# Kernel tuning notes

Measured on AMD Instinct MI355X. Metric: run time of the kernel, lower is better.

The kernel has to match this reference:

```python
import jax, jax.numpy as jnp
import numpy as np

B, S, D = 8, 1024, 1024
H = 16
DK = D // H  # 64, dim_k == dim_v
F = 4096
EPS = 1e-5


def _layernorm(x, w, b):
    mu = jnp.mean(x, axis=-1, keepdims=True)
    var = jnp.mean((x - mu) ** 2, axis=-1, keepdims=True)
    return (x - mu) * jax.lax.rsqrt(var + EPS) * w + b


def setup_inputs() -> dict:
    key = jax.random.key(0)
    ks = jax.random.split(key, 12)
    init = lambda k, shape: (jax.random.normal(k, shape, dtype=jnp.float32) * 0.02)
    return {
        "src": jax.random.normal(ks[0], (B, S, D), dtype=jnp.float32),
        "mask": jnp.zeros((S, S), dtype=jnp.float32),
        # per-head projections, stacked over heads: [H, D, DK]
        "Wq": init(ks[1], (H, D, DK)), "bq": jnp.zeros((H, DK), jnp.float32),
        "Wk": init(ks[2], (H, D, DK)), "bk": jnp.zeros((H, DK), jnp.float32),
        "Wv": init(ks[3], (H, D, DK)), "bv": jnp.zeros((H, DK), jnp.float32),
        "Wo": init(ks[4], (H * DK, D)), "bo": jnp.zeros((D,), jnp.float32),
        "ln1_w": jnp.ones((D,), jnp.float32), "ln1_b": jnp.zeros((D,), jnp.float32),
        "W1": init(ks[5], (D, F)), "b1": jnp.zeros((F,), jnp.float32),
        "W2": init(ks[6], (F, D)), "b2": jnp.zeros((D,), jnp.float32),
        "ln2_w": jnp.ones((D,), jnp.float32), "ln2_b": jnp.zeros((D,), jnp.float32),
    }


def reference(src, mask, Wq, bq, Wk, bk, Wv, bv, Wo, bo,
              ln1_w, ln1_b, W1, b1, W2, b2, ln2_w, ln2_b):
    # per-head projections (vectorized over heads): [B, H, S, DK]
    q = jnp.einsum('bsd,hdk->bhsk', src, Wq) + bq[None, :, None, :]
    k = jnp.einsum('bsd,hdk->bhsk', src, Wk) + bk[None, :, None, :]
    v = jnp.einsum('bsd,hdk->bhsk', src, Wv) + bv[None, :, None, :]
    scale = float(DK) ** 0.5
    logits = jnp.einsum('bhsk,bhtk->bhst', q, k) / scale  # [B,H,S,S]
    logits = logits + mask * (-1e9)
    attn = jax.nn.softmax(logits, axis=-1)
    ctx = jnp.einsum('bhst,bhtv->bhsv', attn, v)  # [B,H,S,DK]
    # concat heads along feature dim (head-major order matches torch cat)
    ctx = jnp.transpose(ctx, (0, 2, 1, 3)).reshape(B, S, H * DK)
    attn_out = ctx @ Wo + bo
    x = _layernorm(src + attn_out, ln1_w, ln1_b)
    ffn = jax.nn.relu(x @ W1 + b1) @ W2 + b2
    return _layernorm(x + ffn, ln2_w, ln2_b)
```

## Files before the change

### kernel.cpp

```cpp
#include <hip/hip_runtime.h>

#define BB 8
#define SS 1024
#define DD 1024
#define HH 16
#define DK 64
#define FF 4096
#define MM (BB*SS)

typedef __attribute__((ext_vector_type(8))) short short8;
typedef __attribute__((ext_vector_type(4))) short short4v;
typedef __attribute__((ext_vector_type(4))) float floatx4;

__device__ inline short f2bf(float f) {
  union { float f; unsigned u; } v; v.f = f;
  unsigned r = (v.u + 0x7FFFu + ((v.u >> 16) & 1u)) >> 16;
  return (short)r;
}
__device__ inline float bf2f(unsigned short u) {
  union { unsigned u; float f; } v; v.u = ((unsigned)u) << 16;
  return v.f;
}

__device__ inline void gload_lds16(const void* g, void* l) {
  __builtin_amdgcn_global_load_lds(
      (const __attribute__((address_space(1))) void*)g,
      (__attribute__((address_space(3))) void*)l, 16, 0, 0);
}

__device__ void tr64(const float* __restrict__ s, unsigned short* __restrict__ d,
                     int R, int C, int r0, int c0, float (*ld)[68], int tid) {
  {
    int r = tid >> 2, c16 = (tid & 3) * 16;
#pragma unroll
    for (int i = 0; i < 4; ++i)
      *(float4*)(&ld[r][c16 + i * 4]) =
          *(const float4*)(s + (size_t)(r0 + r) * C + c0 + c16 + i * 4);
  }
  __syncthreads();
  int c = tid >> 2, r16 = (tid & 3) * 16;
  short8 o0, o1;
#pragma unroll
  for (int i = 0; i < 8; ++i) {
    o0[i] = f2bf(ld[r16 + i][c]);
    o1[i] = f2bf(ld[r16 + 8 + i][c]);
  }
  unsigned short* dp = d + (size_t)(c0 + c) * R + r0 + r16;
  *(short8*)(dp) = o0;
  *(short8*)(dp + 8) = o1;
}

__global__ __launch_bounds__(256) void prep_all(
    const float* __restrict__ src,
    const float* __restrict__ Wq, const float* __restrict__ Wk,
    const float* __restrict__ Wv,
    const float* __restrict__ bq, const float* __restrict__ bk,
    const float* __restrict__ bv, const float* __restrict__ Wo,
    unsigned short* __restrict__ srcb, unsigned short* __restrict__ wqkvT,
    float* __restrict__ bqkv, unsigned short* __restrict__ woT) {
  __shared__ float ld[64][68];
  const int bid = blockIdx.x, tid = threadIdx.x;
  if (bid < 4096) {
    int i8 = (bid * 256 + tid) * 8;
    float4 a = *(const float4*)(src + i8);
    float4 b = *(const float4*)(src + i8 + 4);
    short8 o;
    o[0] = f2bf(a.x); o[1] = f2bf(a.y); o[2] = f2bf(a.z); o[3] = f2bf(a.w);
    o[4] = f2bf(b.x); o[5] = f2bf(b.y); o[6] = f2bf(b.z); o[7] = f2bf(b.w);
    *(short8*)(srcb + i8) = o;
  } else if (bid < 4864) {
    int idx = bid - 4096;
    int d0 = (idx & 15) * 64, h = (idx >> 4) & 15, z = idx >> 8;
    const float* W = (z == 0 ? Wq : z == 1 ? Wk : Wv) + (size_t)h * DD * DK;
    {
      int r = tid >> 2, c16 = (tid & 3) * 16;
#pragma unroll
      for (int i = 0; i < 4; ++i)
        *(float4*)(&ld[r][c16 + i * 4]) =
            *(const float4*)(W + (size_t)(d0 + r) * DK + c16 + i * 4);
    }
    __syncthreads();
    int dv = tid >> 2, d16 = (tid & 3) * 16;
    short8 o0, o1;
#pragma unroll
    for (int i = 0; i < 8; ++i) {
      o0[i] = f2bf(ld[d16 + i][dv]);
      o1[i] = f2bf(ld[d16 + 8 + i][dv]);
    }
    unsigned short* dst = wqkvT + (size_t)(z * 1024 + h * 64 + dv) * DD + d0 + d16;
    *(short8*)(dst) = o0;
    *(short8*)(dst + 8) = o1;
  } else if (bid < 4876) {
    int n = (bid - 4864) * 256 + tid;
    int z = n >> 10;
    const float* s = (z == 0 ? bq : z == 1 ? bk : bv);
    bqkv[n] = s[n & 1023];
  } else {
    int idx = bid - 4876;
    tr64(Wo, woT, 1024, 1024, (idx & 15) * 64, (idx >> 4) * 64, ld, tid);
  }
}

__global__ __launch_bounds__(256) void prep2(
    const unsigned short* __restrict__ qkv, const float* __restrict__ mask,
    const float* __restrict__ W1, const float* __restrict__ W2,
    unsigned short* __restrict__ kbb, unsigned short* __restrict__ vtb,
    unsigned short* __restrict__ maskb, unsigned short* __restrict__ w1T,
    unsigned short* __restrict__ w2T) {
  __shared__ float ldf[64][68];
  const int bid = blockIdx.x, tid = threadIdx.x;
  if (bid < 2048) {
    const int t0 = (bid & 15) * 64, h = (bid >> 4) & 15, b = bid >> 8;
    int row = tid >> 2, c = (tid & 3) * 16;
    const unsigned short* s = qkv + (size_t)(b * SS + t0 + row) * 3072 + 1024 + h * 64 + c;
    unsigned short* d = kbb + ((size_t)((b * HH + h) * SS + t0 + row)) * 64 + c;
    *(short8*)(d) = *(const short8*)(s);
    *(short8*)(d + 8) = *(const short8*)(s + 8);
  } else if (bid < 4096) {
    __shared__ unsigned short ld[64][72];
    const int i = bid - 2048;
    const int t0 = (i & 15) * 64, h = (i >> 4) & 15, b = i >> 8;
    {
      int r = tid >> 2, c16 = (tid & 3) * 16;
      const unsigned short* s = qkv + (size_t)(b * SS + t0 + r) * 3072 + 2048 + h * 64 + c16;
      *(short8*)(&ld[r][c16]) = *(const short8*)(s);
      *(short8*)(&ld[r][c16 + 8]) = *(const short8*)(s + 8);
    }
    __syncthreads();
    int dv = tid >> 2, t16 = (tid & 3) * 16;
    short8 o0, o1;
#pragma unroll
    for (int j = 0; j < 8; ++j) {
      o0[j] = (short)ld[t16 + j][dv];
      o1[j] = (short)ld[t16 + 8 + j][dv];
    }
    unsigned short* d = vtb + ((size_t)(b * HH + h) * DK + dv) * SS + t0 + t16;
    *(short8*)(d) = o0;
    *(short8*)(d + 8) = o1;
  } else if (bid < 4608) {
    int i8 = ((bid - 4096) * 256 + tid) * 8;
    float4 a = *(const float4*)(mask + i8);
    float4 b = *(const float4*)(mask + i8 + 4);
    short8 o;
    o[0] = f2bf(a.x * -1e9f); o[1] = f2bf(a.y * -1e9f);
    o[2] = f2bf(a.z * -1e9f); o[3] = f2bf(a.w * -1e9f);
    o[4] = f2bf(b.x * -1e9f); o[5] = f2bf(b.y * -1e9f);
    o[6] = f2bf(b.z * -1e9f); o[7] = f2bf(b.w * -1e9f);
    *(short8*)(maskb + i8) = o;
  } else if (bid < 5632) {
    int i = bid - 4608;
    tr64(W1, w1T, 1024, 4096, (i & 15) * 64, (i >> 4) * 64, ldf, tid);
  } else {
    int i = bid - 5632;
    tr64(W2, w2T, 4096, 1024, (i & 63) * 64, (i >> 6) * 64, ldf, tid);
  }
}

#define BARE __builtin_amdgcn_s_barrier()
#define VM6  asm volatile("s_waitcnt vmcnt(6)" ::: "memory")
#define VM4  asm volatile("s_waitcnt vmcnt(4)" ::: "memory")
#define VM0  asm volatile("s_waitcnt vmcnt(0)" ::: "memory")
#define PH_HINT asm volatile("s_waitcnt lgkmcnt(8)" ::: "memory")
#define PH_SYNC { \
  __builtin_amdgcn_s_barrier(); \
  asm volatile("s_waitcnt lgkmcnt(0)" ::: "memory"); \
  __builtin_amdgcn_sched_barrier(0); }

#define LOAD_A(lA_, mh_) { \
  _Pragma("unroll") for (int m_ = 0; m_ < 4; ++m_) { \
    const int row_ = wr * 128 + (mh_) * 64 + m_ * 16 + lm; \
    _Pragma("unroll") for (int ks_ = 0; ks_ < 2; ++ks_) \
      a[m_][ks_] = *(const short8*)((lA_) + (size_t)row_ * 64 + \
                     (size_t)(((ks_ * 4 + quad) ^ (lm & 7)) * 8)); \
  } }

#define LOAD_B(lB_, nh_) { \
  _Pragma("unroll") for (int n_ = 0; n_ < 2; ++n_) { \
    const int row_ = wc * 64 + (nh_) * 32 + n_ * 16 + lm; \
    _Pragma("unroll") for (int ks_ = 0; ks_ < 2; ++ks_) \
      bfr[nh_][n_][ks_] = *(const short8*)((lB_) + 16384 + (size_t)row_ * 64 + \
                     (size_t)(((ks_ * 4 + quad) ^ (lm & 7)) * 8)); \
  } }

#define STAGE_A(kt_, mh_, lb_) { \
  _Pragma("unroll") for (int c_ = 0; c_ < 2; ++c_) { \
    const int row_ = c_ * 128 + (mh_) * 64; \
    gload_lds16(gA + (size_t)(kt_) * 64 + (size_t)row_ * K, \
                (lb_) + (size_t)(row_ + wave * 8) * 64); \
  } }

#define STAGE_B(kt_, nh_, lb_) { \
  _Pragma("unroll") for (int c_ = 0; c_ < 2; ++c_) { \
    const int row_ = c_ * 128 + hi128 + (nh_) * 32; \
    gload_lds16(gB + (size_t)(kt_) * 64 + (size_t)row_ * K, \
                (lb_) + 16384 + (size_t)(row_ + (wave & 3) * 8) * 64); \
  } }

#define MFMA_PH(mh_, nh_) { \
  __builtin_amdgcn_s_setprio(1); \
  _Pragma("unroll") for (int m_ = 0; m_ < 4; ++m_) \
    _Pragma("unroll") for (int n_ = 0; n_ < 2; ++n_) { \
      acc[(mh_) * 4 + m_][(nh_) * 2 + n_] = __builtin_amdgcn_mfma_f32_16x16x32_bf16( \
          bfr[nh_][n_][0], a[m_][0], acc[(mh_) * 4 + m_][(nh_) * 2 + n_], 0, 0, 0); \
      acc[(mh_) * 4 + m_][(nh_) * 2 + n_] = __builtin_amdgcn_mfma_f32_16x16x32_bf16( \
          bfr[nh_][n_][1], a[m_][1], acc[(mh_) * 4 + m_][(nh_) * 2 + n_], 0, 0, 0); \
    } \
  __builtin_amdgcn_s_setprio(0); }

#define KITER(e_, ST_) { \
  LOAD_A(buf0, 0); LOAD_B(buf0, 0); \
  STAGE_B((e_) + 1, 1, buf1); \
  PH_HINT; PH_SYNC; MFMA_PH(0, 0); BARE; \
  LOAD_B(buf0, 1); \
  if (ST_) STAGE_A((e_) + 2, 0, buf0); \
  PH_SYNC; MFMA_PH(0, 1); BARE; \
  LOAD_A(buf0, 1); \
  if (ST_) STAGE_B((e_) + 2, 0, buf0); \
  PH_SYNC; MFMA_PH(1, 0); BARE; \
  if (ST_) STAGE_A((e_) + 2, 1, buf0); \
  PH_SYNC; MFMA_PH(1, 1); \
  if (ST_) { VM6; } else { VM0; } \
  BARE; \
  LOAD_A(buf1, 0); LOAD_B(buf1, 0); \
  if (ST_) STAGE_B((e_) + 2, 1, buf0); \
  PH_HINT; PH_SYNC; MFMA_PH(0, 0); BARE; \
  LOAD_B(buf1, 1); \
  if (ST_) STAGE_A((e_) + 3, 0, buf1); \
  PH_SYNC; MFMA_PH(0, 1); BARE; \
  LOAD_A(buf1, 1); \
  if (ST_) STAGE_B((e_) + 3, 0, buf1); \
  PH_SYNC; MFMA_PH(1, 0); BARE; \
  if (ST_) { \
    STAGE_A((e_) + 3, 1, buf1); \
    PH_SYNC; MFMA_PH(1, 1); VM6; BARE; \
  } else { \
    PH_SYNC; MFMA_PH(1, 1); \
  } }

template <int RELU>
__global__ __launch_bounds__(512, 2) void gemm256(
    const unsigned short* __restrict__ A, const unsigned short* __restrict__ Bt,
    const float* __restrict__ bias, unsigned short* __restrict__ C,
    int M, int N, int K) {
  extern __shared__ unsigned short lds[];
  unsigned short* buf0 = lds;
  unsigned short* buf1 = lds + 32768;
  const int tid = threadIdx.x;
  const int wave = tid >> 6, lane = tid & 63;
  const int lm = lane & 15, quad = lane >> 4;
  const int wr = wave >> 2, wc = wave & 3;

  const int nwg = gridDim.x;
  const int cpx = nwg >> 3;
  const int id = (blockIdx.x & 7) * cpx + (blockIdx.x >> 3);
  const int nbx = N >> 8;
  const int bx = id % nbx, by = id / nbx;
  const int n0 = bx << 8, m0 = by << 8;

  const int NT = K >> 6;

  const int srow = tid >> 3;
  const int chs = (tid & 7) ^ (srow & 7);
  const int hi128 = (tid >= 256) ? 64 : 0;
  const int r32 = (tid >> 3) & 31;
  const unsigned short* gA = A + (size_t)(m0 + srow) * K + chs * 8;
  const unsigned short* gB = Bt + (size_t)(n0 + r32) * K + chs * 8;

  floatx4 acc[8][4] = {};
  short8 a[4][2], bfr[2][2][2];

  STAGE_A(0, 0, buf0); STAGE_B(0, 0, buf0);
  STAGE_A(0, 1, buf0); STAGE_B(0, 1, buf0);
  STAGE_A(1, 0, buf1); STAGE_B(1, 0, buf1);
  STAGE_A(1, 1, buf1);
  VM6;
  BARE;

  const int TT = NT >> 1;
  for (int i = 0; i < TT - 1; ++i) {
    KITER(2 * i, 1);
  }
  KITER(NT - 2, 0);

#pragma unroll
  for (int mi = 0; mi < 8; ++mi) {
    const int row = m0 + wr * 128 + mi * 16 + lm;
#pragma unroll
    for (int nj = 0; nj < 4; ++nj) {
      const int col = n0 + wc * 64 + nj * 16 + (quad << 2);
      const float4 bv = *(const float4*)(bias + col);
      float vv[4] = {acc[mi][nj][0] + bv.x, acc[mi][nj][1] + bv.y,
                     acc[mi][nj][2] + bv.z, acc[mi][nj][3] + bv.w};
      short4v o;
#pragma unroll
      for (int r = 0; r < 4; ++r) {
        float v = vv[r];
        if (RELU) v = fmaxf(v, 0.f);
        o[r] = f2bf(v);
      }
      *(short4v*)(C + (size_t)row * N + col) = o;
    }
  }
}

#define LOAD_A1(lb_, mh_) { \
  _Pragma("unroll") for (int m_ = 0; m_ < 2; ++m_) { \
    const int row_ = wr * 64 + (mh_) * 32 + m_ * 16 + lm; \
    _Pragma("unroll") for (int ks_ = 0; ks_ < 2; ++ks_) \
      a[m_][ks_] = *(const short8*)((lb_) + (size_t)row_ * 64 + \
                     (size_t)(((ks_ * 4 + quad) ^ (lm & 7)) * 8)); \
  } }

#define LOAD_B1(lb_, nh_) { \
  _Pragma("unroll") for (int n_ = 0; n_ < 2; ++n_) { \
    const int row_ = wc * 64 + (nh_) * 32 + n_ * 16 + lm; \
    _Pragma("unroll") for (int ks_ = 0; ks_ < 2; ++ks_) \
      bfr[nh_][n_][ks_] = *(const short8*)((lb_) + 8192 + (size_t)row_ * 64 + \
                     (size_t)(((ks_ * 4 + quad) ^ (lm & 7)) * 8)); \
  } }

#define STAGE_A1(kt_, mh_, lb_) { \
  gload_lds16(gA + (size_t)(kt_) * 64 + (size_t)((mh_) * 32) * K, \
              (lb_) + (size_t)((mh_) * 32 + hi128 + (wave & 3) * 8) * 64); }

#define STAGE_B1(kt_, nh_, lb_) { \
  _Pragma("unroll") for (int c_ = 0; c_ < 2; ++c_) { \
    const int row_ = c_ * 128 + hi128 + (nh_) * 32; \
    gload_lds16(gB + (size_t)(kt_) * 64 + (size_t)row_ * K, \
                (lb_) + 8192 + (size_t)(row_ + (wave & 3) * 8) * 64); \
  } }

#define MFMA_PH1(mh_, nh_) { \
  __builtin_amdgcn_s_setprio(1); \
  _Pragma("unroll") for (int m_ = 0; m_ < 2; ++m_) \
    _Pragma("unroll") for (int n_ = 0; n_ < 2; ++n_) { \
      acc[(mh_) * 2 + m_][(nh_) * 2 + n_] = __builtin_amdgcn_mfma_f32_16x16x32_bf16( \
          bfr[nh_][n_][0], a[m_][0], acc[(mh_) * 2 + m_][(nh_) * 2 + n_], 0, 0, 0); \
      acc[(mh_) * 2 + m_][(nh_) * 2 + n_] = __builtin_amdgcn_mfma_f32_16x16x32_bf16( \
          bfr[nh_][n_][1], a[m_][1], acc[(mh_) * 2 + m_][(nh_) * 2 + n_], 0, 0, 0); \
    } \
  __builtin_amdgcn_s_setprio(0); }

#define KITER1(e_, ST_) { \
  LOAD_A1(buf0, 0); LOAD_B1(buf0, 0); \
  STAGE_B1((e_) + 1, 1, buf1); \
  PH_SYNC; MFMA_PH1(0, 0); BARE; \
  LOAD_B1(buf0, 1); \
  if (ST_) STAGE_A1((e_) + 2, 0, buf0); \
  PH_SYNC; MFMA_PH1(0, 1); BARE; \
  LOAD_A1(buf0, 1); \
  if (ST_) STAGE_B1((e_) + 2, 0, buf0); \
  PH_SYNC; MFMA_PH1(1, 0); BARE; \
  if (ST_) STAGE_A1((e_) + 2, 1, buf0); \
  PH_SYNC; MFMA_PH1(1, 1); \
  if (ST_) { VM4; } else { VM0; } \
  BARE; \
  LOAD_A1(buf1, 0); LOAD_B1(buf1, 0); \
  if (ST_) STAGE_B1((e_) + 2, 1, buf0); \
  PH_SYNC; MFMA_PH1(0, 0); BARE; \
  LOAD_B1(buf1, 1); \
  if (ST_) STAGE_A1((e_) + 3, 0, buf1); \
  PH_SYNC; MFMA_PH1(0, 1); BARE; \
  LOAD_A1(buf1, 1); \
  if (ST_) STAGE_B1((e_) + 3, 0, buf1); \
  PH_SYNC; MFMA_PH1(1, 0); BARE; \
  if (ST_) { \
    STAGE_A1((e_) + 3, 1, buf1); \
    PH_SYNC; MFMA_PH1(1, 1); VM4; BARE; \
  } else { \
    PH_SYNC; MFMA_PH1(1, 1); \
  } }

__global__ __launch_bounds__(512, 2) void gemm128(
    const unsigned short* __restrict__ A, const unsigned short* __restrict__ Bt,
    const float* __restrict__ bias, unsigned short* __restrict__ C,
    int M, int N, int K) {
  extern __shared__ unsigned short lds[];
  unsigned short* buf0 = lds;
  unsigned short* buf1 = lds + 24576;
  const int tid = threadIdx.x;
  const int wave = tid >> 6, lane = tid & 63;
  const int lm = lane & 15, quad = lane >> 4;
  const int wr = wave >> 2, wc = wave & 3;

  const int nwg = gridDim.x;
  const int cpx = nwg >> 3;
  const int id = (blockIdx.x & 7) * cpx + (blockIdx.x >> 3);
  const int nbx = N >> 8;
  const int bx = id % nbx, by = id / nbx;
  const int n0 = bx << 8, m0 = by << 7;

  const int NT = K >> 6;

  const int srow = tid >> 3;
  const int chs = (tid & 7) ^ (srow & 7);
  const int hi128 = (tid >= 256) ? 64 : 0;
  const int r32 = (tid >> 3) & 31;
  const unsigned short* gA = A + (size_t)(m0 + hi128 + r32) * K + chs * 8;
  const unsigned short* gB = Bt + (size_t)(n0 + r32) * K + chs * 8;

  floatx4 acc[4][4] = {};
  short8 a[2][2], bfr[2][2][2];

  STAGE_A1(0, 0, buf0); STAGE_B1(0, 0, buf0);
  STAGE_A1(0, 1, buf0); STAGE_B1(0, 1, buf0);
  STAGE_A1(1, 0, buf1); STAGE_B1(1, 0, buf1);
  STAGE_A1(1, 1, buf1);
  VM4;
  BARE;

  const int TT = NT >> 1;
  for (int i = 0; i < TT - 1; ++i) {
    KITER1(2 * i, 1);
  }
  KITER1(NT - 2, 0);

#pragma unroll
  for (int mi = 0; mi < 4; ++mi) {
    const int row = m0 + wr * 64 + mi * 16 + lm;
#pragma unroll
    for (int nj = 0; nj < 4; ++nj) {
      const int col = n0 + wc * 64 + nj * 16 + (quad << 2);
      const float4 bv = *(const float4*)(bias + col);
      short4v o;
      o[0] = f2bf(acc[mi][nj][0] + bv.x);
      o[1] = f2bf(acc[mi][nj][1] + bv.y);
      o[2] = f2bf(acc[mi][nj][2] + bv.z);
      o[3] = f2bf(acc[mi][nj][3] + bv.w);
      *(short4v*)(C + (size_t)row * N + col) = o;
    }
  }
}

__global__ __launch_bounds__(512) void attention_flash(
    const unsigned short* __restrict__ qkv, const unsigned short* __restrict__ kb,
    const unsigned short* __restrict__ vt, const unsigned short* __restrict__ maskb,
    unsigned short* __restrict__ ctx) {
  const int flat = blockIdx.x;
  const int bh = (flat & 7) + 8 * (flat >> 6);
  const int qt = (flat >> 3) & 7;
  const int b = bh >> 4, h = bh & 15;
  const int s0 = qt * 128;
  const int tid = threadIdx.x;
  const int wave = tid >> 6, lane = tid & 63;
  const int lm = lane & 15, quad = lane >> 4;

  __shared__ __align__(16) unsigned short Ks[64 * 64];
  __shared__ __align__(16) unsigned short Vs[64 * 64];
  __shared__ __align__(16) unsigned short Ms[128 * 64];
  __shared__ __align__(16) unsigned short Ps[8][16 * 72];

  const unsigned short* qp = qkv + (size_t)(b * SS + s0 + wave * 16 + lm) * 3072 + h * 64;
  const short8 qa0 = *(const short8*)(qp + quad * 8);
  const short8 qa1 = *(const short8*)(qp + quad * 8 + 32);

  const unsigned short* kbase = kb + (size_t)bh * SS * DK;
  const unsigned short* vbase = vt + (size_t)bh * DK * SS;
  const unsigned short* mbase = maskb + (size_t)s0 * SS;

  const int sr = lane >> 3, sj = lane & 7;
  float m_run = -3e38f, l_run = 0.f;
  floatx4 O[4] = {};

  for (int it = 0; it < 16; ++it) {
    const int t0 = it * 64;
    __syncthreads();
    {
      int r = wave * 8 + sr;
      gload_lds16(kbase + (size_t)(t0 + r) * 64 + (size_t)(sj ^ (r & 7)) * 8,
                  (char*)Ks + wave * 1024);
      gload_lds16(vbase + (size_t)r * SS + t0 + (size_t)(sj ^ (r & 7)) * 8,
                  (char*)Vs + wave * 1024);
      int q1 = wave * 8 + sr;
      gload_lds16(mbase + (size_t)q1 * SS + t0 + (size_t)(sj ^ (q1 & 7)) * 8,
                  (char*)Ms + wave * 1024);
      int q2 = 64 + wave * 8 + sr;
      gload_lds16(mbase + (size_t)q2 * SS + t0 + (size_t)(sj ^ (q2 & 7)) * 8,
                  (char*)Ms + 8192 + wave * 1024);
    }
    __syncthreads();

    float p[16];
    float mt = -3e38f;
    const int qr = wave * 16 + lm;
#pragma unroll
    for (int ts = 0; ts < 4; ++ts) {
      int r = ts * 16 + lm;
      short8 kf0 = *(const short8*)&Ks[(r * 8 + (quad ^ (r & 7))) * 8];
      short8 kf1 = *(const short8*)&Ks[(r * 8 + ((quad + 4) ^ (r & 7))) * 8];
      floatx4 c = {0.f, 0.f, 0.f, 0.f};
      c = __builtin_amdgcn_mfma_f32_16x16x32_bf16(kf0, qa0, c, 0, 0, 0);
      c = __builtin_amdgcn_mfma_f32_16x16x32_bf16(kf1, qa1, c, 0, 0, 0);
      int mj = (ts * 2 + (quad >> 1)) ^ (qr & 7);
      short4v mv = *(const short4v*)&Ms[(qr * 8 + mj) * 8 + (quad & 1) * 4];
#pragma unroll
      for (int r2 = 0; r2 < 4; ++r2) {
        float sv = c[r2] * 0.125f + bf2f((unsigned short)mv[r2]);
        p[ts * 4 + r2] = sv;
        mt = fmaxf(mt, sv);
      }
    }
    mt = fmaxf(mt, __shfl_xor(mt, 16));
    mt = fmaxf(mt, __shfl_xor(mt, 32));
    float mnew = fmaxf(m_run, mt);
    float alpha = __expf(m_run - mnew);
    float psum = 0.f;
#pragma unroll
    for (int i = 0; i < 16; ++i) { p[i] = __expf(p[i] - mnew); psum += p[i]; }
    psum += __shfl_xor(psum, 16);
    psum += __shfl_xor(psum, 32);
    l_run = l_run * alpha + psum;
    m_run = mnew;
#pragma unroll
    for (int d = 0; d < 4; ++d)
#pragma unroll
      for (int r2 = 0; r2 < 4; ++r2) O[d][r2] *= alpha;

    unsigned short* pw = &Ps[wave][lm * 72];
#pragma unroll
    for (int ts = 0; ts < 4; ++ts) {
      short4v pv4;
#pragma unroll
      for (int r2 = 0; r2 < 4; ++r2) pv4[r2] = f2bf(p[ts * 4 + r2]);
      *(short4v*)(pw + ts * 16 + quad * 4) = pv4;
    }

#pragma unroll
    for (int ks = 0; ks < 2; ++ks) {
      short8 pf = *(const short8*)(pw + ks * 32 + quad * 8);
#pragma unroll
      for (int d = 0; d < 4; ++d) {
        int dv = d * 16 + lm;
        short8 vf = *(const short8*)&Vs[(dv * 8 + ((ks * 4 + quad) ^ (dv & 7))) * 8];
        O[d] = __builtin_amdgcn_mfma_f32_16x16x32_bf16(vf, pf, O[d], 0, 0, 0);
      }
    }
  }

  const float inv = 1.f / l_run;
  unsigned short* cp = ctx + (size_t)(b * SS + s0 + wave * 16 + lm) * DD + h * 64;
#pragma unroll
  for (int d = 0; d < 4; ++d) {
    short4v o;
#pragma unroll
    for (int r2 = 0; r2 < 4; ++r2) o[r2] = f2bf(O[d][r2] * inv);
    *(short4v*)(cp + d * 16 + quad * 4) = o;
  }
}

template <int A_BF16, int OUT_BF16>
__global__ __launch_bounds__(256) void residual_ln(
    const void* __restrict__ a_, const unsigned short* __restrict__ rr,
    const float* __restrict__ w, const float* __restrict__ bias,
    void* __restrict__ out_) {
  const int row = blockIdx.x;
  const int t = threadIdx.x;
  float x[4];
  if (A_BF16) {
    short4v va = *(const short4v*)((const unsigned short*)a_ + (size_t)row * DD + t * 4);
#pragma unroll
    for (int i = 0; i < 4; ++i) x[i] = bf2f((unsigned short)va[i]);
  } else {
    float4 va = *(const float4*)((const float*)a_ + (size_t)row * DD + t * 4);
    x[0] = va.x; x[1] = va.y; x[2] = va.z; x[3] = va.w;
  }
  {
    short4v vr = *(const short4v*)(rr + (size_t)row * DD + t * 4);
#pragma unroll
    for (int i = 0; i < 4; ++i) x[i] += bf2f((unsigned short)vr[i]);
  }
  float s = 0.f, ss = 0.f;
#pragma unroll
  for (int i = 0; i < 4; ++i) { s += x[i]; ss += x[i] * x[i]; }
#pragma unroll
  for (int o = 32; o > 0; o >>= 1) {
    s  += __shfl_down(s, o);
    ss += __shfl_down(ss, o);
  }
  __shared__ float2 sred[4];
  int wid = t >> 6;
  if ((t & 63) == 0) sred[wid] = make_float2(s, ss);
  __syncthreads();
  float st = 0.f, sst = 0.f;
#pragma unroll
  for (int i = 0; i < 4; ++i) { st += sred[i].x; sst += sred[i].y; }
  float mu  = st * (1.f / 1024.f);
  float var = sst * (1.f / 1024.f) - mu * mu;
  float rsq = rsqrtf(var + 1e-5f);
  float4 vw = *(const float4*)(w + t * 4);
  float4 vb = *(const float4*)(bias + t * 4);
  float o[4];
  o[0] = (x[0] - mu) * rsq * vw.x + vb.x;
  o[1] = (x[1] - mu) * rsq * vw.y + vb.y;
  o[2] = (x[2] - mu) * rsq * vw.z + vb.z;
  o[3] = (x[3] - mu) * rsq * vw.w + vb.w;
  if (OUT_BF16) {
    short4v ov;
#pragma unroll
    for (int i = 0; i < 4; ++i) ov[i] = f2bf(o[i]);
    *(short4v*)((unsigned short*)out_ + (size_t)row * DD + t * 4) = ov;
  } else {
    float4 ov = {o[0], o[1], o[2], o[3]};
    *(float4*)((float*)out_ + (size_t)row * DD + t * 4) = ov;
  }
}

extern "C" void kernel_launch(void* const* d_in, const int* in_sizes, int n_in,
                              void* d_out, int out_size, void* d_ws, size_t ws_size,
                              hipStream_t stream) {
  const float* src  = (const float*)d_in[0];
  const float* mask = (const float*)d_in[1];
  const float* Wq = (const float*)d_in[2];  const float* bq = (const float*)d_in[3];
  const float* Wk = (const float*)d_in[4];  const float* bk = (const float*)d_in[5];
  const float* Wv = (const float*)d_in[6];  const float* bv = (const float*)d_in[7];
  const float* Wo = (const float*)d_in[8];  const float* bo = (const float*)d_in[9];
  const float* ln1w = (const float*)d_in[10]; const float* ln1b = (const float*)d_in[11];
  const float* W1 = (const float*)d_in[12]; const float* b1 = (const float*)d_in[13];
  const float* W2 = (const float*)d_in[14]; const float* b2 = (const float*)d_in[15];
  const float* ln2w = (const float*)d_in[16]; const float* ln2b = (const float*)d_in[17];
  float* out = (float*)d_out;

  const size_t NEED = 125841408;
  if (ws_size < NEED) return;

  char* ws = (char*)d_ws;
  unsigned short* qkv   = (unsigned short*)(ws);
  unsigned short* vtb   = (unsigned short*)(ws + 50331648);
  unsigned short* kbb   = (unsigned short*)(ws + 67108864);
  unsigned short* ctxb  = (unsigned short*)(ws + 83886080);
  unsigned short* srcb  = (unsigned short*)(ws + 100663296);
  unsigned short* w1T   = (unsigned short*)(ws + 100663296);
  unsigned short* w2T   = (unsigned short*)(ws + 109051904);
  unsigned short* wqkvT = (unsigned short*)(ws + 117440512);
  unsigned short* maskb = (unsigned short*)(ws + 117440512);
  unsigned short* woT   = (unsigned short*)(ws + 123731968);
  float*          bqkv  = (float*)(ws + 125829120);
  unsigned short* h1       = qkv;
  unsigned short* attn_out = kbb;
  unsigned short* xb       = ctxb;
  unsigned short* ffn      = kbb;

  static bool lds_init = false;
  if (!lds_init) {
    auto* k0 = gemm256<0>;
    auto* k1 = gemm256<1>;
    hipFuncSetAttribute((const void*)k0, hipFuncAttributeMaxDynamicSharedMemorySize, 131072);
    hipFuncSetAttribute((const void*)k1, hipFuncAttributeMaxDynamicSharedMemorySize, 131072);
    hipFuncSetAttribute((const void*)gemm128, hipFuncAttributeMaxDynamicSharedMemorySize, 98304);
    lds_init = true;
  }

  prep_all<<<5132, 256, 0, stream>>>(src, Wq, Wk, Wv, bq, bk, bv, Wo,
                                     srcb, wqkvT, bqkv, woT);
  gemm128<<<(3072 / 256) * (MM / 128), 512, 98304, stream>>>(srcb, wqkvT, bqkv, qkv, MM, 3072, DD);
  prep2<<<6656, 256, 0, stream>>>(qkv, mask, W1, W2, kbb, vtb, maskb, w1T, w2T);
  attention_flash<<<1024, 512, 0, stream>>>(qkv, kbb, vtb, maskb, ctxb);
  gemm128<<<(DD / 256) * (MM / 128), 512, 98304, stream>>>(ctxb, woT, bo, attn_out, MM, DD, DD);
  residual_ln<0, 1><<<MM, 256, 0, stream>>>(src, attn_out, ln1w, ln1b, xb);
  gemm256<1><<<(FF / 256) * (MM / 256), 512, 131072, stream>>>(xb, w1T, b1, h1, MM, FF, DD);
  gemm128<<<(DD / 256) * (MM / 128), 512, 98304, stream>>>(h1, w2T, b2, ffn, MM, DD, FF);
  residual_ln<1, 0><<<MM, 256, 0, stream>>>(xb, ffn, ln2w, ln2b, out);
}
```

Baseline: 519.9 us.

## Double-buffer K/V tiles, load mask to registers, lazy softmax rescale in attention

The flash-attention loop now double-buffers K and V in LDS and prefetches the next tile while the current one is computed, so one barrier per iteration replaces two. The mask is read straight from global memory into registers with a one-tile prefetch instead of being staged through LDS. The running-max rescale of the output accumulator is skipped unless the max grows by more than a threshold, and the bf16 packing uses a packed convert instruction. These changes add LDS footprint and register pressure, and the lazy rescale depends on the exp values staying bounded.

```diff
diff --git a/kernel.cpp b/kernel.cpp
--- a/kernel.cpp
+++ b/kernel.cpp
@@ -432,6 +432,63 @@
   }
 }
 
+#define ATT_ITER(IT, CB, MU, MN) { \
+  const int t0a = (IT) * 64; \
+  if ((IT) + 1 < 16) { \
+    gload_lds16(ksrc + (size_t)((IT) + 1) * 4096, (char*)Ks[(CB) ^ 1] + wave * 1024); \
+    gload_lds16(vsrc + ((IT) + 1) * 64, (char*)Vs[(CB) ^ 1] + wave * 1024); \
+    _Pragma("unroll") for (int ts = 0; ts < 4; ++ts) \
+      MN[ts] = *(const short4v*)(mrow + t0a + 64 + ts * 16 + quad * 4); \
+  } \
+  __builtin_amdgcn_sched_barrier(0); \
+  float p[16]; \
+  float mt = -3e38f; \
+  _Pragma("unroll") for (int ts = 0; ts < 4; ++ts) { \
+    int rr = ts * 16 + lm; \
+    short8 kf0 = *(const short8*)&Ks[CB][(rr * 8 + (quad ^ (rr & 7))) * 8]; \
+    short8 kf1 = *(const short8*)&Ks[CB][(rr * 8 + ((quad + 4) ^ (rr & 7))) * 8]; \
+    floatx4 c = {0.f, 0.f, 0.f, 0.f}; \
+    c = __builtin_amdgcn_mfma_f32_16x16x32_bf16(kf0, qa0, c, 0, 0, 0); \
+    c = __builtin_amdgcn_mfma_f32_16x16x32_bf16(kf1, qa1, c, 0, 0, 0); \
+    _Pragma("unroll") for (int r2 = 0; r2 < 4; ++r2) { \
+      float sv = c[r2] * 0.125f + bf2f((unsigned short)MU[ts][r2]); \
+      p[ts * 4 + r2] = sv; \
+      mt = fmaxf(mt, sv); \
+    } \
+  } \
+  mt = fmaxf(mt, __shfl_xor(mt, 16)); \
+  mt = fmaxf(mt, __shfl_xor(mt, 32)); \
+  if (!__all(mt - m_run <= 8.f)) { \
+    float mnew = fmaxf(m_run, mt); \
+    float alpha = __expf(m_run - mnew); \
+    _Pragma("unroll") for (int d = 0; d < 4; ++d) \
+      _Pragma("unroll") for (int r2 = 0; r2 < 4; ++r2) O[d][r2] *= alpha; \
+    l_run *= alpha; \
+    m_run = mnew; \
+  } \
+  float psum = 0.f; \
+  _Pragma("unroll") for (int i = 0; i < 16; ++i) { p[i] = __expf(p[i] - m_run); psum += p[i]; } \
+  psum += __shfl_xor(psum, 16); \
+  psum += __shfl_xor(psum, 32); \
+  l_run += psum; \
+  _Pragma("unroll") for (int ts = 0; ts < 4; ++ts) { \
+    unsigned plo, phi; \
+    asm("v_cvt_pk_bf16_f32 %0, %1, %2" : "=v"(plo) : "v"(p[ts * 4 + 0]), "v"(p[ts * 4 + 1])); \
+    asm("v_cvt_pk_bf16_f32 %0, %1, %2" : "=v"(phi) : "v"(p[ts * 4 + 2]), "v"(p[ts * 4 + 3])); \
+    uint2 pu; pu.x = plo; pu.y = phi; \
+    *(uint2*)(pw + ts * 16 + quad * 4) = pu; \
+  } \
+  _Pragma("unroll") for (int ks = 0; ks < 2; ++ks) { \
+    short8 pf = *(const short8*)(pw + ks * 32 + quad * 8); \
+    _Pragma("unroll") for (int d = 0; d < 4; ++d) { \
+      int dv = d * 16 + lm; \
+      short8 vf = *(const short8*)&Vs[CB][(dv * 8 + ((ks * 4 + quad) ^ (dv & 7))) * 8]; \
+      O[d] = __builtin_amdgcn_mfma_f32_16x16x32_bf16(vf, pf, O[d], 0, 0, 0); \
+    } \
+  } \
+  __syncthreads(); \
+}
+
 __global__ __launch_bounds__(512) void attention_flash(
     const unsigned short* __restrict__ qkv, const unsigned short* __restrict__ kb,
     const unsigned short* __restrict__ vt, const unsigned short* __restrict__ maskb,
@@ -445,9 +502,8 @@
   const int wave = tid >> 6, lane = tid & 63;
   const int lm = lane & 15, quad = lane >> 4;
 
-  __shared__ __align__(16) unsigned short Ks[64 * 64];
-  __shared__ __align__(16) unsigned short Vs[64 * 64];
-  __shared__ __align__(16) unsigned short Ms[128 * 64];
+  __shared__ __align__(16) unsigned short Ks[2][64 * 64];
+  __shared__ __align__(16) unsigned short Vs[2][64 * 64];
   __shared__ __align__(16) unsigned short Ps[8][16 * 72];
 
   const unsigned short* qp = qkv + (size_t)(b * SS + s0 + wave * 16 + lm) * 3072 + h * 64;
@@ -456,85 +512,28 @@
 
   const unsigned short* kbase = kb + (size_t)bh * SS * DK;
   const unsigned short* vbase = vt + (size_t)bh * DK * SS;
-  const unsigned short* mbase = maskb + (size_t)s0 * SS;
+  const unsigned short* mrow = maskb + (size_t)(s0 + wave * 16 + lm) * SS;
 
   const int sr = lane >> 3, sj = lane & 7;
+  const int srr = wave * 8 + sr;
+  const unsigned short* ksrc = kbase + (size_t)srr * 64 + (size_t)(sj ^ (srr & 7)) * 8;
+  const unsigned short* vsrc = vbase + (size_t)srr * SS + (size_t)(sj ^ (srr & 7)) * 8;
+
+  unsigned short* pw = &Ps[wave][lm * 72];
   float m_run = -3e38f, l_run = 0.f;
   floatx4 O[4] = {};
-
-  for (int it = 0; it < 16; ++it) {
-    const int t0 = it * 64;
-    __syncthreads();
-    {
-      int r = wave * 8 + sr;
-      gload_lds16(kbase + (size_t)(t0 + r) * 64 + (size_t)(sj ^ (r & 7)) * 8,
-                  (char*)Ks + wave * 1024);
-      gload_lds16(vbase + (size_t)r * SS + t0 + (size_t)(sj ^ (r & 7)) * 8,
-                  (char*)Vs + wave * 1024);
-      int q1 = wave * 8 + sr;
-      gload_lds16(mbase + (size_t)q1 * SS + t0 + (size_t)(sj ^ (q1 & 7)) * 8,
-                  (char*)Ms + wave * 1024);
-      int q2 = 64 + wave * 8 + sr;
-      gload_lds16(mbase + (size_t)q2 * SS + t0 + (size_t)(sj ^ (q2 & 7)) * 8,
-                  (char*)Ms + 8192 + wave * 1024);
-    }
-    __syncthreads();
-
-    float p[16];
-    float mt = -3e38f;
-    const int qr = wave * 16 + lm;
-#pragma unroll
-    for (int ts = 0; ts < 4; ++ts) {
-      int r = ts * 16 + lm;
-      short8 kf0 = *(const short8*)&Ks[(r * 8 + (quad ^ (r & 7))) * 8];
-      short8 kf1 = *(const short8*)&Ks[(r * 8 + ((quad + 4) ^ (r & 7))) * 8];
-      floatx4 c = {0.f, 0.f, 0.f, 0.f};
-      c = __builtin_amdgcn_mfma_f32_16x16x32_bf16(kf0, qa0, c, 0, 0, 0);
-      c = __builtin_amdgcn_mfma_f32_16x16x32_bf16(kf1, qa1, c, 0, 0, 0);
-      int mj = (ts * 2 + (quad >> 1)) ^ (qr & 7);
-      short4v mv = *(const short4v*)&Ms[(qr * 8 + mj) * 8 + (quad & 1) * 4];
-#pragma unroll
-      for (int r2 = 0; r2 < 4; ++r2) {
-        float sv = c[r2] * 0.125f + bf2f((unsigned short)mv[r2]);
-        p[ts * 4 + r2] = sv;
-        mt = fmaxf(mt, sv);
-      }
-    }
-    mt = fmaxf(mt, __shfl_xor(mt, 16));
-    mt = fmaxf(mt, __shfl_xor(mt, 32));
-    float mnew = fmaxf(m_run, mt);
-    float alpha = __expf(m_run - mnew);
-    float psum = 0.f;
-#pragma unroll
-    for (int i = 0; i < 16; ++i) { p[i] = __expf(p[i] - mnew); psum += p[i]; }
-    psum += __shfl_xor(psum, 16);
-    psum += __shfl_xor(psum, 32);
-    l_run = l_run * alpha + psum;
-    m_run = mnew;
-#pragma unroll
-    for (int d = 0; d < 4; ++d)
-#pragma unroll
-      for (int r2 = 0; r2 < 4; ++r2) O[d][r2] *= alpha;
-
-    unsigned short* pw = &Ps[wave][lm * 72];
-#pragma unroll
-    for (int ts = 0; ts < 4; ++ts) {
-      short4v pv4;
-#pragma unroll
-      for (int r2 = 0; r2 < 4; ++r2) pv4[r2] = f2bf(p[ts * 4 + r2]);
-      *(short4v*)(pw + ts * 16 + quad * 4) = pv4;
-    }
-
-#pragma unroll
-    for (int ks = 0; ks < 2; ++ks) {
-      short8 pf = *(const short8*)(pw + ks * 32 + quad * 8);
-#pragma unroll
-      for (int d = 0; d < 4; ++d) {
-        int dv = d * 16 + lm;
-        short8 vf = *(const short8*)&Vs[(dv * 8 + ((ks * 4 + quad) ^ (dv & 7))) * 8];
-        O[d] = __builtin_amdgcn_mfma_f32_16x16x32_bf16(vf, pf, O[d], 0, 0, 0);
-      }
-    }
+  short4v mvA[4], mvB[4];
+
+  gload_lds16(ksrc, (char*)Ks[0] + wave * 1024);
+  gload_lds16(vsrc, (char*)Vs[0] + wave * 1024);
+#pragma unroll
+  for (int ts = 0; ts < 4; ++ts)
+    mvA[ts] = *(const short4v*)(mrow + ts * 16 + quad * 4);
+  __syncthreads();
+
+  for (int it2 = 0; it2 < 16; it2 += 2) {
+    ATT_ITER(it2, 0, mvA, mvB);
+    ATT_ITER(it2 + 1, 1, mvB, mvA);
   }
 
   const float inv = 1.f / l_run;
```

After: 514.3 us. No clear change (-1.1%).
